# Performance work log

Measured on AMD Instinct MI355X. Metric: run time of the kernel, lower is better.

The kernel has to match this reference:

```python
import jax, jax.numpy as jnp
import numpy as np

B, S, D, H, DFF, G = 2, 2048, 1024, 16, 4096, 64
HD = D // H  # seq_dimensions = d_model // num_heads
SCALE = 1.0 / np.sqrt(HD).astype(np.float32)


def _ln(x, g, b):
    m = x.mean(-1, keepdims=True)
    v = x.var(-1, keepdims=True)
    return (x - m) / jnp.sqrt(v + 1e-5) * g + b


def _mha(q_in, k_in, v_in, wq, bq, wk, bk, wv, bv, wo, bo, mask):
    Bq, Sq, _ = q_in.shape
    Sk = k_in.shape[1]
    def proj(t, w, b):
        return (t @ w + b).reshape(t.shape[0], t.shape[1], H, HD).transpose(0, 2, 1, 3)
    q = proj(q_in, wq, bq)  # [B,H,Sq,HD]
    k = proj(k_in, wk, bk)
    v = proj(v_in, wv, bv)
    scores = jnp.einsum('bhqd,bhkd->bhqk', q, k) * SCALE
    if mask is not None:
        scores = jnp.where(mask, scores, jnp.float32(-1e9))
    a = jax.nn.softmax(scores, axis=-1)
    o = jnp.einsum('bhqk,bhkd->bhqd', a, v).transpose(0, 2, 1, 3).reshape(Bq, Sq, D)
    return o @ wo + bo


def setup_inputs() -> dict:
    key = jax.random.key(0)
    ks = jax.random.split(key, 32)
    w = lambda i, shape: jax.random.normal(ks[i], shape, jnp.float32) * 0.02
    z = lambda shape: jnp.zeros(shape, jnp.float32)
    # BigBird-style mask: causal + global (first G tokens) + G random cols per row
    rng = np.random.default_rng(0)
    mask = np.tril(np.ones((S, S), dtype=bool))
    mask[:, :G] = True
    mask[:G, :] = True
    rand_cols = rng.integers(0, S, size=(S, G))
    mask[np.arange(S)[:, None], rand_cols] = True
    return dict(
        cur_input=jax.random.normal(ks[0], (B, S, D), jnp.float32),
        classVector=jax.random.normal(ks[1], (B, 1, 10), jnp.float32),
        attn_mask=jnp.asarray(mask),
        sa_wq=w(2, (D, D)), sa_bq=z(D), sa_wk=w(3, (D, D)), sa_bk=z(D),
        sa_wv=w(4, (D, D)), sa_bv=z(D), sa_wo=w(5, (D, D)), sa_bo=z(D),
        ln1_g=jnp.ones(D, jnp.float32), ln1_b=z(D),
        ce_w=w(6, (10, D)), ce_b=z(D),
        ca_wq=w(7, (D, D)), ca_bq=z(D), ca_wk=w(8, (D, D)), ca_bk=z(D),
        ca_wv=w(9, (D, D)), ca_bv=z(D), ca_wo=w(10, (D, D)), ca_bo=z(D),
        ln2_g=jnp.ones(D, jnp.float32), ln2_b=z(D),
        ff_w1=w(11, (D, DFF)), ff_b1=z(DFF), ff_w2=w(12, (DFF, D)), ff_b2=z(D),
        ln3_g=jnp.ones(D, jnp.float32), ln3_b=z(D),
    )


def reference(cur_input, classVector, attn_mask,
              sa_wq, sa_bq, sa_wk, sa_bk, sa_wv, sa_bv, sa_wo, sa_bo, ln1_g, ln1_b,
              ce_w, ce_b,
              ca_wq, ca_bq, ca_wk, ca_bk, ca_wv, ca_bv, ca_wo, ca_bo, ln2_g, ln2_b,
              ff_w1, ff_b1, ff_w2, ff_b2, ln3_g, ln3_b):
    # AddNorm(masked rand+global self-attn)
    sa = _mha(cur_input, cur_input, cur_input,
              sa_wq, sa_bq, sa_wk, sa_bk, sa_wv, sa_bv, sa_wo, sa_bo, attn_mask)
    h = _ln(cur_input + sa, ln1_g, ln1_b)
    # class vector embedding -> cross-attn K/V
    cv = classVector @ ce_w + ce_b  # [B,1,D]
    ca = _mha(h, cv, cv, ca_wq, ca_bq, ca_wk, ca_bk, ca_wv, ca_bv, ca_wo, ca_bo, None)
    h2 = _ln(h + ca, ln2_g, ln2_b)
    # AddNorm(FFN)
    ff = jax.nn.relu(h2 @ ff_w1 + ff_b1) @ ff_w2 + ff_b2
    return _ln(h2 + ff, ln3_g, ln3_b)
```

## Files before the change

### kernel.cpp

```cpp
#include <hip/hip_runtime.h>
#include <hip/hip_bf16.h>
#include <stdint.h>

#define S_LEN 2048
#define DMODEL 1024
#define NHEAD 16
#define BATCH 2

typedef __bf16 bf16x8 __attribute__((ext_vector_type(8)));
typedef __bf16 bf16x4 __attribute__((ext_vector_type(4)));
typedef float f32x4 __attribute__((ext_vector_type(4)));

__device__ __forceinline__ void gll16(const void* gsrc, void* ldst) {
  auto g = (const __attribute__((address_space(1))) unsigned int*)(uintptr_t)gsrc;
  auto l = (__attribute__((address_space(3))) unsigned int*)(uint32_t)(uintptr_t)ldst;
  __builtin_amdgcn_global_load_lds(g, l, 16, 0, 0);
}

__device__ __forceinline__ void wt_core(const float* __restrict__ W, __bf16* __restrict__ Wt,
                                        int Kd, int Nd, int bx, int by) {
  __shared__ __bf16 tile[64 * 72];
  const int n0 = bx * 64, k0 = by * 64;
  const int t = threadIdx.x;
#pragma unroll
  for (int i = 0; i < 16; ++i) {
    int idx = t + 256 * i;
    int r = idx >> 6, c = idx & 63;
    tile[r * 72 + c] = (__bf16)W[(size_t)(k0 + r) * Nd + n0 + c];
  }
  __syncthreads();
#pragma unroll
  for (int i = 0; i < 2; ++i) {
    int ch = t + 256 * i;
    int r = ch >> 3, c0 = (ch & 7) * 8;
    bf16x8 v;
#pragma unroll
    for (int j = 0; j < 8; ++j) v[j] = tile[(c0 + j) * 72 + r];
    *(bf16x8*)&Wt[(size_t)(n0 + r) * Kd + k0 + c0] = v;
  }
}

__global__ __launch_bounds__(256) void prep_kernel(
    const uint8_t* __restrict__ m8, unsigned long long* __restrict__ mb, const float* w0,
    const float* w1, const float* w2, const float* w3, __bf16* o0, __bf16* o1, __bf16* o2,
    __bf16* o3, const float* fw1, const float* fw2, __bf16* fo1, __bf16* fo2,
    const float* __restrict__ x, __bf16* __restrict__ y) {
  const int bid = blockIdx.x;
  const int t = threadIdx.x;
  if (bid < 256) {
    const int idx = bid * 256 + t;
    const int r = idx >> 5, c = idx & 31;
    const bool u8 = (m8[1] != 0);
    unsigned long long bits = 0;
    if (u8) {
      const unsigned long long* p = (const unsigned long long*)(m8 + (size_t)r * 2048 + c * 64);
#pragma unroll
      for (int i = 0; i < 8; ++i) {
        unsigned long long wq = p[i];
#pragma unroll
        for (int j = 0; j < 8; ++j)
          if ((wq >> (8 * j)) & 0xFFull) bits |= 1ull << (i * 8 + j);
      }
    } else {
      const int* p = (const int*)m8 + (size_t)r * 2048 + (size_t)c * 64;
#pragma unroll
      for (int i = 0; i < 64; ++i)
        if (p[i] != 0) bits |= 1ull << i;
    }
    mb[(size_t)r * 32 + c] = bits;
  } else if (bid < 1280) {
    const int local = bid - 256;
    const int z = local >> 8, lb = local & 255;
    const float* W = (z == 0) ? w0 : (z == 1) ? w1 : (z == 2) ? w2 : w3;
    __bf16* Wt = (z == 0) ? o0 : (z == 1) ? o1 : (z == 2) ? o2 : o3;
    wt_core(W, Wt, 1024, 1024, lb & 15, lb >> 4);
  } else if (bid < 2304) {
    const int lb = bid - 1280;
    wt_core(fw1, fo1, 1024, 4096, lb & 63, lb >> 6);
  } else if (bid < 3328) {
    const int lb = bid - 2304;
    wt_core(fw2, fo2, 4096, 1024, lb >> 6, lb & 63);
  } else {
    const int lb = bid - 3328;
#pragma unroll
    for (int j = 0; j < 4; ++j) {
      int i = lb * 1024 + j * 256 + t;
      float4 v = ((const float4*)x)[i];
      bf16x4 o = {(__bf16)v.x, (__bf16)v.y, (__bf16)v.z, (__bf16)v.w};
      *(bf16x4*)(y + (size_t)i * 4) = o;
    }
  }
}

__device__ __forceinline__ void gemm_core(const __bf16* __restrict__ A,
                                          const __bf16* __restrict__ Bt,
                                          const float* __restrict__ bias,
                                          float* __restrict__ outF, __bf16* __restrict__ outB,
                                          bool relu, float scale, int N, int K) {
  __shared__ __bf16 As[2][128 * 64];
  __shared__ __bf16 Bs[2][128 * 64];
  const int t = threadIdx.x;
  const int l = t & 63, w = t >> 6;
  const int wr = w >> 1, wc = w & 1;
  const int gx = gridDim.x;
  const int lin = blockIdx.x + gx * blockIdx.y;
  const int cpx = (gx * gridDim.y) >> 3;
  const int s = (lin & 7) * cpx + (lin >> 3);
  const int bx = s % gx, by = s / gx;
  const int l15 = l & 15, l4 = l >> 4;
  f32x4 acc[4][4] = {};
  const size_t arow = (size_t)by * 128;
  const size_t brow = (size_t)bx * 128;

  auto stage = [&](int d, int k0) {
#pragma unroll
    for (int i = 0; i < 4; ++i) {
      int c = t + 256 * i;
      int r = c >> 3, sl = c & 7;
      int kk = (sl ^ (r & 7)) << 3;
      gll16(A + (arow + r) * K + k0 + kk, (char*)As[d] + (size_t)c * 16);
      gll16(Bt + (brow + r) * K + k0 + kk, (char*)Bs[d] + (size_t)c * 16);
    }
  };

  stage(0, 0);
  asm volatile("s_waitcnt vmcnt(0)" ::: "memory");
  __builtin_amdgcn_s_barrier();
  int cur = 0;
  for (int k0 = 0; k0 < K; k0 += 64) {
    if (k0 + 64 < K) stage(cur ^ 1, k0 + 64);
#pragma unroll
    for (int kk = 0; kk < 2; ++kk) {
      bf16x8 af[4], bfr[4];
#pragma unroll
      for (int m = 0; m < 4; ++m) {
        int row = wr * 64 + m * 16 + l15, vs = kk * 4 + l4;
        af[m] = *(const bf16x8*)((char*)As[cur] + row * 128 + ((vs ^ (row & 7)) << 4));
      }
#pragma unroll
      for (int n = 0; n < 4; ++n) {
        int row = wc * 64 + n * 16 + l15, vs = kk * 4 + l4;
        bfr[n] = *(const bf16x8*)((char*)Bs[cur] + row * 128 + ((vs ^ (row & 7)) << 4));
      }
#pragma unroll
      for (int m = 0; m < 4; ++m)
#pragma unroll
        for (int n = 0; n < 4; ++n)
          acc[m][n] = __builtin_amdgcn_mfma_f32_16x16x32_bf16(af[m], bfr[n], acc[m][n], 0, 0, 0);
    }
    asm volatile("s_waitcnt vmcnt(0)" ::: "memory");
    __builtin_amdgcn_s_barrier();
    cur ^= 1;
  }
  const int r0 = by * 128 + wr * 64, c0 = bx * 128 + wc * 64;
#pragma unroll
  for (int m = 0; m < 4; ++m) {
#pragma unroll
    for (int n = 0; n < 4; ++n) {
      int col = c0 + n * 16 + l15;
      float bv = bias ? bias[col] : 0.0f;
#pragma unroll
      for (int i = 0; i < 4; ++i) {
        int row = r0 + m * 16 + l4 * 4 + i;
        float v = (acc[m][n][i] + bv) * scale;
        if (relu) v = fmaxf(v, 0.0f);
        if (outF) outF[(size_t)row * N + col] = v;
        if (outB) outB[(size_t)row * N + col] = (__bf16)v;
      }
    }
  }
}

__global__ __launch_bounds__(256) void gemm_kernel(const __bf16* A, const __bf16* Bt,
                                                   const float* bias, float* outF, __bf16* outB,
                                                   int relu, float scale, int N, int K) {
  gemm_core(A, Bt, bias, outF, outB, relu != 0, scale, N, K);
}

__global__ __launch_bounds__(256) void gemm64_kernel(const __bf16* __restrict__ A,
                                                     const __bf16* __restrict__ Bt,
                                                     const float* __restrict__ bias,
                                                     float* __restrict__ outF,
                                                     __bf16* __restrict__ outB, int relu,
                                                     int N, int K) {
  __shared__ __bf16 As[2][128 * 64];
  __shared__ __bf16 Bs[2][64 * 64];
  const int t = threadIdx.x;
  const int l = t & 63, w = t >> 6;
  const int gx = gridDim.x;
  const int lin = blockIdx.x + gx * blockIdx.y;
  const int cpx = (gx * gridDim.y) >> 3;
  const int s = (lin & 7) * cpx + (lin >> 3);
  const int bx = s % gx, by = s / gx;
  const int l15 = l & 15, l4 = l >> 4;
  f32x4 acc[2][4] = {};
  const size_t arow = (size_t)by * 128;
  const size_t brow = (size_t)bx * 64;

  auto stage = [&](int d, int k0) {
#pragma unroll
    for (int i = 0; i < 4; ++i) {
      int c = t + 256 * i;
      int r = c >> 3, sl = c & 7;
      int kk = (sl ^ (r & 7)) << 3;
      gll16(A + (arow + r) * K + k0 + kk, (char*)As[d] + (size_t)c * 16);
    }
#pragma unroll
    for (int i = 0; i < 2; ++i) {
      int c = t + 256 * i;
      int r = c >> 3, sl = c & 7;
      int kk = (sl ^ (r & 7)) << 3;
      gll16(Bt + (brow + r) * K + k0 + kk, (char*)Bs[d] + (size_t)c * 16);
    }
  };

  stage(0, 0);
  asm volatile("s_waitcnt vmcnt(0)" ::: "memory");
  __builtin_amdgcn_s_barrier();
  int cur = 0;
  for (int k0 = 0; k0 < K; k0 += 64) {
    if (k0 + 64 < K) stage(cur ^ 1, k0 + 64);
#pragma unroll
    for (int kk = 0; kk < 2; ++kk) {
      bf16x8 af[2], bfr[4];
#pragma unroll
      for (int m = 0; m < 2; ++m) {
        int row = w * 32 + m * 16 + l15, vs = kk * 4 + l4;
        af[m] = *(const bf16x8*)((char*)As[cur] + row * 128 + ((vs ^ (row & 7)) << 4));
      }
#pragma unroll
      for (int n = 0; n < 4; ++n) {
        int row = n * 16 + l15, vs = kk * 4 + l4;
        bfr[n] = *(const bf16x8*)((char*)Bs[cur] + row * 128 + ((vs ^ (row & 7)) << 4));
      }
#pragma unroll
      for (int m = 0; m < 2; ++m)
#pragma unroll
        for (int n = 0; n < 4; ++n)
          acc[m][n] = __builtin_amdgcn_mfma_f32_16x16x32_bf16(af[m], bfr[n], acc[m][n], 0, 0, 0);
    }
    asm volatile("s_waitcnt vmcnt(0)" ::: "memory");
    __builtin_amdgcn_s_barrier();
    cur ^= 1;
  }
  const int r0 = by * 128 + w * 32, c0 = bx * 64;
#pragma unroll
  for (int m = 0; m < 2; ++m) {
#pragma unroll
    for (int n = 0; n < 4; ++n) {
      int col = c0 + n * 16 + l15;
      float bv = bias ? bias[col] : 0.0f;
#pragma unroll
      for (int i = 0; i < 4; ++i) {
        int row = r0 + m * 16 + l4 * 4 + i;
        float v = acc[m][n][i] + bv;
        if (relu) v = fmaxf(v, 0.0f);
        if (outF) outF[(size_t)row * N + col] = v;
        if (outB) outB[(size_t)row * N + col] = (__bf16)v;
      }
    }
  }
}

__global__ __launch_bounds__(256) void gemm_qkv_kernel(const __bf16* __restrict__ A,
                                                       const __bf16* __restrict__ WT3,
                                                       const float* bq, const float* bk,
                                                       const float* bv, __bf16* Qo, __bf16* Ko,
                                                       __bf16* Vo) {
  __shared__ __bf16 As[2][128 * 64];
  __shared__ __bf16 Bs[2][128 * 64];
  const int t = threadIdx.x;
  const int l = t & 63, w = t >> 6;
  const int wr = w >> 1, wc = w & 1;
  const int gx = gridDim.x;
  const int lin = blockIdx.x + gx * blockIdx.y;
  const int cpx = (gx * gridDim.y) >> 3;
  const int s = (lin & 7) * cpx + (lin >> 3);
  const int bx = s % gx, by = s / gx;
  const int l15 = l & 15, l4 = l >> 4;
  const int K = 1024;
  f32x4 acc[4][4] = {};
  const size_t arow = (size_t)by * 128;
  const size_t brow = (size_t)bx * 128;

  auto stage = [&](int d, int k0) {
#pragma unroll
    for (int i = 0; i < 4; ++i) {
      int c = t + 256 * i;
      int r = c >> 3, sl = c & 7;
      int kk = (sl ^ (r & 7)) << 3;
      gll16(A + (arow + r) * K + k0 + kk, (char*)As[d] + (size_t)c * 16);
      gll16(WT3 + (brow + r) * K + k0 + kk, (char*)Bs[d] + (size_t)c * 16);
    }
  };

  stage(0, 0);
  asm volatile("s_waitcnt vmcnt(0)" ::: "memory");
  __builtin_amdgcn_s_barrier();
  int cur = 0;
  for (int k0 = 0; k0 < K; k0 += 64) {
    if (k0 + 64 < K) stage(cur ^ 1, k0 + 64);
#pragma unroll
    for (int kk = 0; kk < 2; ++kk) {
      bf16x8 af[4], bfr[4];
#pragma unroll
      for (int m = 0; m < 4; ++m) {
        int row = wr * 64 + m * 16 + l15, vs = kk * 4 + l4;
        af[m] = *(const bf16x8*)((char*)As[cur] + row * 128 + ((vs ^ (row & 7)) << 4));
      }
#pragma unroll
      for (int n = 0; n < 4; ++n) {
        int row = wc * 64 + n * 16 + l15, vs = kk * 4 + l4;
        bfr[n] = *(const bf16x8*)((char*)Bs[cur] + row * 128 + ((vs ^ (row & 7)) << 4));
      }
#pragma unroll
      for (int m = 0; m < 4; ++m)
#pragma unroll
        for (int n = 0; n < 4; ++n)
          acc[m][n] = __builtin_amdgcn_mfma_f32_16x16x32_bf16(af[m], bfr[n], acc[m][n], 0, 0, 0);
    }
    asm volatile("s_waitcnt vmcnt(0)" ::: "memory");
    __builtin_amdgcn_s_barrier();
    cur ^= 1;
  }
  const int z = bx >> 3;
  __bf16* out = (z == 0) ? Qo : (z == 1) ? Ko : Vo;
  const float* bias = (z == 0) ? bq : (z == 1) ? bk : bv;
  const float scale = (z == 0) ? 0.125f : 1.0f;
  const int r0 = by * 128 + wr * 64, c0 = (bx & 7) * 128 + wc * 64;
#pragma unroll
  for (int m = 0; m < 4; ++m) {
#pragma unroll
    for (int n = 0; n < 4; ++n) {
      int col = c0 + n * 16 + l15;
      float bvv = bias[col];
#pragma unroll
      for (int i = 0; i < 4; ++i) {
        int row = r0 + m * 16 + l4 * 4 + i;
        out[(size_t)row * DMODEL + col] = (__bf16)((acc[m][n][i] + bvv) * scale);
      }
    }
  }
}

__global__ __launch_bounds__(256) void vt_kernel(const __bf16* __restrict__ V,
                                                 __bf16* __restrict__ Vt) {
  __shared__ __bf16 tile[64 * 72];
  const int sb = blockIdx.x, h = blockIdx.y, b = blockIdx.z;
  const int t = threadIdx.x;
#pragma unroll
  for (int i = 0; i < 2; ++i) {
    int ch = t + 256 * i;
    int r = ch >> 3, c0 = (ch & 7) * 8;
    *(bf16x8*)&tile[r * 72 + c0] =
        *(const bf16x8*)&V[(size_t)(b * S_LEN + sb * 64 + r) * DMODEL + h * 64 + c0];
  }
  __syncthreads();
#pragma unroll
  for (int i = 0; i < 2; ++i) {
    int ch = t + 256 * i;
    int r = ch >> 3, c0 = (ch & 7) * 8;
    bf16x8 v;
#pragma unroll
    for (int j = 0; j < 8; ++j) v[j] = tile[(c0 + j) * 72 + r];
    *(bf16x8*)&Vt[((size_t)((b * NHEAD + h) * 64) + r) * S_LEN + sb * 64 + c0] = v;
  }
}

__global__ __launch_bounds__(256, 4) void flash_kernel(const __bf16* __restrict__ Q,
                                                       const __bf16* __restrict__ K,
                                                       const __bf16* __restrict__ Vt,
                                                       const unsigned long long* __restrict__ mbits,
                                                       __bf16* __restrict__ O) {
  __shared__ char smem[40 * 1024];
  const int lin = blockIdx.x + 32 * (blockIdx.y + 16 * blockIdx.z);
  const int xr = lin & 7, xm = lin >> 3;
  const int g = xr + 8 * (xm & 3);
  const int qb = xm >> 2;
  const int h = g & 15, b = g >> 4;
  const int t = threadIdx.x, w = t >> 6, l = t & 63;
  const int l15 = l & 15, l4 = l >> 4;
  const int q_glob = qb * 64 + w * 16 + l15;

#pragma unroll
  for (int i = 0; i < 2; ++i) {
    int c = t + 256 * i;
    int r = c >> 3, p = c & 7;
    int vsl = p ^ (r & 7);
    gll16(Q + (size_t)(b * S_LEN + qb * 64 + r) * DMODEL + h * 64 + vsl * 8,
          smem + (size_t)c * 16);
    gll16(K + (size_t)(b * S_LEN + r) * DMODEL + h * 64 + vsl * 8, smem + 8192 + (size_t)c * 16);
    gll16(Vt + (size_t)((b * NHEAD + h) * 64 + r) * S_LEN + vsl * 8, smem + 24576 + (size_t)c * 16);
  }
  __syncthreads();

  bf16x8 aq[2];
#pragma unroll
  for (int ks = 0; ks < 2; ++ks) {
    int row = w * 16 + l15, vs = ks * 4 + l4;
    aq[ks] = *(const bf16x8*)(smem + row * 128 + ((vs ^ (row & 7)) << 4));
  }
  char* PsW = smem + w * 2048;

  f32x4 o[4] = {};
  float mrow = -INFINITY, lrow = 0.f;
  unsigned long long mb_cur = 0, mb_next = 0;
  int cur = 0;
  for (int kt = 0; kt < 32; ++kt) {
    char* Kc = smem + 8192 + cur * 8192;
    char* Vc = smem + 24576 + cur * 8192;
    if (kt < 31) {
      char* Kn = smem + 8192 + (cur ^ 1) * 8192;
      char* Vn = smem + 24576 + (cur ^ 1) * 8192;
#pragma unroll
      for (int i = 0; i < 2; ++i) {
        int c = t + 256 * i;
        int r = c >> 3, p = c & 7;
        int vsl = p ^ (r & 7);
        gll16(K + (size_t)(b * S_LEN + (kt + 1) * 64 + r) * DMODEL + h * 64 + vsl * 8,
              Kn + (size_t)c * 16);
        gll16(Vt + (size_t)((b * NHEAD + h) * 64 + r) * S_LEN + (kt + 1) * 64 + vsl * 8,
              Vn + (size_t)c * 16);
      }
      mb_next = mbits[(size_t)q_glob * 32 + kt + 1];
    }
    f32x4 s[4] = {};
    __builtin_amdgcn_s_setprio(1);
#pragma unroll
    for (int ks = 0; ks < 2; ++ks)
#pragma unroll
      for (int n = 0; n < 4; ++n) {
        int row = n * 16 + l15, vs = ks * 4 + l4;
        bf16x8 kf = *(const bf16x8*)(Kc + row * 128 + ((vs ^ (row & 7)) << 4));
        s[n] = __builtin_amdgcn_mfma_f32_16x16x32_bf16(kf, aq[ks], s[n], 0, 0, 0);
      }
    __builtin_amdgcn_s_setprio(0);
    const bool skip = (kt < qb) || (kt == 0) || (qb == 0);
    float tmax = s[0][0];
#pragma unroll
    for (int n = 0; n < 4; ++n)
#pragma unroll
      for (int i = 0; i < 4; ++i) tmax = fmaxf(tmax, s[n][i]);
    tmax = fmaxf(tmax, __shfl_xor(tmax, 16));
    tmax = fmaxf(tmax, __shfl_xor(tmax, 32));
    if (__ballot(tmax > mrow)) {
      const float nm = fmaxf(mrow, tmax);
      const float alpha = __expf(mrow - nm);
      mrow = nm;
      lrow *= alpha;
#pragma unroll
      for (int i = 0; i < 4; ++i) {
        float ai = __shfl(alpha, (l & 48) | (l4 * 4 + i));
#pragma unroll
        for (int n = 0; n < 4; ++n) o[n][i] *= ai;
      }
    }
    float pv[4][4];
#pragma unroll
    for (int n = 0; n < 4; ++n)
#pragma unroll
      for (int i = 0; i < 4; ++i) pv[n][i] = __expf(s[n][i] - mrow);
    if (!skip) {
#pragma unroll
      for (int n = 0; n < 4; ++n) {
        unsigned int mB = (unsigned int)(mb_cur >> (n * 16 + l4 * 4));
#pragma unroll
        for (int i = 0; i < 4; ++i)
          if (!((mB >> i) & 1)) pv[n][i] = 0.f;
      }
    }
    float tsum = 0.f;
#pragma unroll
    for (int n = 0; n < 4; ++n)
#pragma unroll
      for (int i = 0; i < 4; ++i) tsum += pv[n][i];
    tsum += __shfl_xor(tsum, 16);
    tsum += __shfl_xor(tsum, 32);
    lrow += tsum;
#pragma unroll
    for (int n = 0; n < 4; ++n) {
      bf16x4 pk = {(__bf16)pv[n][0], (__bf16)pv[n][1], (__bf16)pv[n][2], (__bf16)pv[n][3]};
      int slot = n * 4 + l4;
      *(bf16x4*)(PsW + l15 * 128 + ((slot ^ l15) & 15) * 8) = pk;
    }
#pragma unroll
    for (int ks = 0; ks < 2; ++ks) {
      int s0 = (ks * 8 + l4 * 2) ^ l15;
      int s1 = (ks * 8 + l4 * 2 + 1) ^ l15;
      bf16x4 pa0 = *(const bf16x4*)(PsW + l15 * 128 + (s0 & 15) * 8);
      bf16x4 pa1 = *(const bf16x4*)(PsW + l15 * 128 + (s1 & 15) * 8);
      bf16x8 ap = {pa0[0], pa0[1], pa0[2], pa0[3], pa1[0], pa1[1], pa1[2], pa1[3]};
      __builtin_amdgcn_s_setprio(1);
#pragma unroll
      for (int n = 0; n < 4; ++n) {
        int vrow = n * 16 + l15, vvs = ks * 4 + l4;
        bf16x8 bv = *(const bf16x8*)(Vc + vrow * 128 + ((vvs ^ (vrow & 7)) << 4));
        o[n] = __builtin_amdgcn_mfma_f32_16x16x32_bf16(ap, bv, o[n], 0, 0, 0);
      }
      __builtin_amdgcn_s_setprio(0);
    }
    asm volatile("s_waitcnt vmcnt(0)" ::: "memory");
    __builtin_amdgcn_s_barrier();
    mb_cur = mb_next;
    cur ^= 1;
  }
#pragma unroll
  for (int i = 0; i < 4; ++i) {
    float li = __shfl(lrow, (l & 48) | (l4 * 4 + i));
    float rli = 1.0f / li;
#pragma unroll
    for (int n = 0; n < 4; ++n)
      O[(size_t)(b * S_LEN + qb * 64 + w * 16 + l4 * 4 + i) * DMODEL + h * 64 + n * 16 + l15] =
          (__bf16)(o[n][i] * rli);
  }
}

__global__ __launch_bounds__(256) void ln_kernel(const float* __restrict__ x,
                                                 const float* __restrict__ res,
                                                 const float* __restrict__ resvec,
                                                 const float* __restrict__ g,
                                                 const float* __restrict__ beta,
                                                 float* __restrict__ outF,
                                                 __bf16* __restrict__ outB) {
  const int row = blockIdx.x;
  const int b = row >> 11;
  const int t = threadIdx.x;
  float4 v = ((const float4*)(x + (size_t)row * DMODEL))[t];
  if (res) {
    float4 r = ((const float4*)(res + (size_t)row * DMODEL))[t];
    v.x += r.x; v.y += r.y; v.z += r.z; v.w += r.w;
  }
  if (resvec) {
    float4 r = ((const float4*)(resvec + (size_t)b * DMODEL))[t];
    v.x += r.x; v.y += r.y; v.z += r.z; v.w += r.w;
  }
  float s1 = v.x + v.y + v.z + v.w;
  float s2 = v.x * v.x + v.y * v.y + v.z * v.z + v.w * v.w;
#pragma unroll
  for (int off = 32; off; off >>= 1) {
    s1 += __shfl_xor(s1, off);
    s2 += __shfl_xor(s2, off);
  }
  __shared__ float red[8];
  const int w = t >> 6, l = t & 63;
  if (l == 0) { red[w] = s1; red[4 + w] = s2; }
  __syncthreads();
  s1 = red[0] + red[1] + red[2] + red[3];
  s2 = red[4] + red[5] + red[6] + red[7];
  const float mean = s1 * (1.0f / DMODEL);
  const float var = s2 * (1.0f / DMODEL) - mean * mean;
  const float rstd = rsqrtf(var + 1e-5f);
  float4 gg = ((const float4*)g)[t];
  float4 bb = ((const float4*)beta)[t];
  float4 o;
  o.x = (v.x - mean) * rstd * gg.x + bb.x;
  o.y = (v.y - mean) * rstd * gg.y + bb.y;
  o.z = (v.z - mean) * rstd * gg.z + bb.z;
  o.w = (v.w - mean) * rstd * gg.w + bb.w;
  if (outF) ((float4*)(outF + (size_t)row * DMODEL))[t] = o;
  if (outB) {
    bf16x4 p = {(__bf16)o.x, (__bf16)o.y, (__bf16)o.z, (__bf16)o.w};
    *(bf16x4*)(outB + (size_t)row * DMODEL + t * 4) = p;
  }
}

__global__ __launch_bounds__(256) void matvec_part_kernel(const float* __restrict__ x,
                                                          const float* __restrict__ W,
                                                          float* __restrict__ part,
                                                          const float* __restrict__ cls,
                                                          const float* __restrict__ cw,
                                                          const float* __restrict__ cb) {
  const int c = blockIdx.x, b = blockIdx.y;
  const int t = threadIdx.x;
  const int k0 = c * 16;
  __shared__ float xs[16];
  if (cls) {
    if (t < 16) {
      float s = cb[k0 + t];
#pragma unroll
      for (int j = 0; j < 10; ++j) s += cls[b * 10 + j] * cw[j * DMODEL + k0 + t];
      xs[t] = s;
    }
  } else {
    if (t < 16) xs[t] = x[b * DMODEL + k0 + t];
  }
  __syncthreads();
  float4 acc = {0.f, 0.f, 0.f, 0.f};
#pragma unroll
  for (int k = 0; k < 16; ++k) {
    float xv = xs[k];
    float4 wv = ((const float4*)(W + (size_t)(k0 + k) * DMODEL))[t];
    acc.x += xv * wv.x; acc.y += xv * wv.y; acc.z += xv * wv.z; acc.w += xv * wv.w;
  }
  ((float4*)(part + ((size_t)(b * 64 + c)) * DMODEL))[t] = acc;
}

__global__ __launch_bounds__(256) void matvec_red_kernel(const float* __restrict__ part,
                                                         const float* __restrict__ bias,
                                                         float* __restrict__ out) {
  const int b = blockIdx.y;
  const int t = threadIdx.x;
  float4 acc = ((const float4*)bias)[t];
#pragma unroll 8
  for (int c = 0; c < 64; ++c) {
    float4 p = ((const float4*)(part + ((size_t)(b * 64 + c)) * DMODEL))[t];
    acc.x += p.x; acc.y += p.y; acc.z += p.z; acc.w += p.w;
  }
  ((float4*)(out + (size_t)b * DMODEL))[t] = acc;
}

extern "C" void kernel_launch(void* const* d_in, const int* in_sizes, int n_in, void* d_out,
                              int out_size, void* d_ws, size_t ws_size, hipStream_t stream) {
  (void)in_sizes; (void)n_in; (void)out_size; (void)ws_size;
  const float* cur = (const float*)d_in[0];
  const float* cls = (const float*)d_in[1];
  const uint8_t* msk = (const uint8_t*)d_in[2];
  const float* sa_wq = (const float*)d_in[3];
  const float* sa_bq = (const float*)d_in[4];
  const float* sa_wk = (const float*)d_in[5];
  const float* sa_bk = (const float*)d_in[6];
  const float* sa_wv = (const float*)d_in[7];
  const float* sa_bv = (const float*)d_in[8];
  const float* sa_wo = (const float*)d_in[9];
  const float* sa_bo = (const float*)d_in[10];
  const float* ln1_g = (const float*)d_in[11];
  const float* ln1_b = (const float*)d_in[12];
  const float* ce_w = (const float*)d_in[13];
  const float* ce_b = (const float*)d_in[14];
  const float* ca_wv = (const float*)d_in[19];
  const float* ca_bv = (const float*)d_in[20];
  const float* ca_wo = (const float*)d_in[21];
  const float* ca_bo = (const float*)d_in[22];
  const float* ln2_g = (const float*)d_in[23];
  const float* ln2_b = (const float*)d_in[24];
  const float* ff_w1 = (const float*)d_in[25];
  const float* ff_b1 = (const float*)d_in[26];
  const float* ff_w2 = (const float*)d_in[27];
  const float* ff_b2 = (const float*)d_in[28];
  const float* ln3_g = (const float*)d_in[29];
  const float* ln3_b = (const float*)d_in[30];

  char* ws = (char*)d_ws;
  const size_t MB = 1ull << 20;
  __bf16* WQT = (__bf16*)(ws + 0 * MB);
  __bf16* WKT = (__bf16*)(ws + 2 * MB);
  __bf16* WVT = (__bf16*)(ws + 4 * MB);
  __bf16* WOT = (__bf16*)(ws + 6 * MB);
  __bf16* W1T = (__bf16*)(ws + 8 * MB);
  __bf16* W2T = (__bf16*)(ws + 16 * MB);
  __bf16* XBF = (__bf16*)(ws + 24 * MB);
  __bf16* QBF = (__bf16*)(ws + 32 * MB);
  __bf16* KBF = (__bf16*)(ws + 40 * MB);
  __bf16* VBF = (__bf16*)(ws + 48 * MB);
  __bf16* VTT = (__bf16*)(ws + 56 * MB);
  __bf16* F1 = (__bf16*)(ws + 32 * MB);
  float* ATT = (float*)(ws + 64 * MB);
  float* HF = (float*)(ws + 80 * MB);
  float* H2F = (float*)(ws + 96 * MB);
  __bf16* H2B = (__bf16*)(ws + 112 * MB);
  float* VV = (float*)(ws + 120 * MB);
  float* CAV = (float*)(ws + 120 * MB + 65536);
  unsigned long long* MBITS = (unsigned long long*)(ws + 121 * MB);
  float* MVP = (float*)(ws + 122 * MB);

  dim3 blk(256);
  prep_kernel<<<dim3(4352), blk, 0, stream>>>(msk, MBITS, sa_wq, sa_wk, sa_wv, sa_wo, WQT, WKT,
                                              WVT, WOT, ff_w1, ff_w2, W1T, W2T, cur, XBF);
  gemm_qkv_kernel<<<dim3(24, 32), blk, 0, stream>>>(XBF, WQT, sa_bq, sa_bk, sa_bv, QBF, KBF, VBF);
  vt_kernel<<<dim3(32, 16, 2), blk, 0, stream>>>(VBF, VTT);
  flash_kernel<<<dim3(32, 16, 2), blk, 0, stream>>>(QBF, KBF, VTT, MBITS, XBF);
  gemm64_kernel<<<dim3(16, 32), blk, 0, stream>>>(XBF, WOT, sa_bo, ATT, nullptr, 0, 1024, 1024);
  ln_kernel<<<dim3(4096), blk, 0, stream>>>(cur, ATT, nullptr, ln1_g, ln1_b, HF, nullptr);
  matvec_part_kernel<<<dim3(64, 2), blk, 0, stream>>>(nullptr, ca_wv, MVP, cls, ce_w, ce_b);
  matvec_red_kernel<<<dim3(1, 2), blk, 0, stream>>>(MVP, ca_bv, VV);
  matvec_part_kernel<<<dim3(64, 2), blk, 0, stream>>>(VV, ca_wo, MVP, nullptr, nullptr, nullptr);
  matvec_red_kernel<<<dim3(1, 2), blk, 0, stream>>>(MVP, ca_bo, CAV);
  ln_kernel<<<dim3(4096), blk, 0, stream>>>(HF, nullptr, CAV, ln2_g, ln2_b, H2F, H2B);
  gemm_kernel<<<dim3(32, 32), blk, 0, stream>>>(H2B, W1T, ff_b1, nullptr, F1, 1, 1.0f, 4096, 1024);
  gemm64_kernel<<<dim3(16, 32), blk, 0, stream>>>(F1, W2T, ff_b2, ATT, nullptr, 0, 1024, 4096);
  ln_kernel<<<dim3(4096), blk, 0, stream>>>(H2F, ATT, nullptr, ln3_g, ln3_b, (float*)d_out,
                                            nullptr);
}
```

Baseline: 296.2 us.

## Use exp2 softmax with MFMA row sums and fold cross-attn matvecs into prep

The Q scale now includes log2(e), so the flash kernel can use the raw v_exp_f32 (exp2) instruction in place of __expf. The softmax denominator is accumulated by an extra MFMA against a ones vector instead of shuffle-based row sums. The cross-attention class-vector embedding and the first matvec stage move into prep_kernel as extra blocks, and the first reduction is fused into the second matvec, removing two launches. The trade-offs are one extra MFMA per tile, and a row sum taken from bf16-rounded probabilities rather than the fp32 values.

```diff
diff --git a/kernel.cpp b/kernel.cpp
--- a/kernel.cpp
+++ b/kernel.cpp
@@ -17,6 +17,12 @@
   __builtin_amdgcn_global_load_lds(g, l, 16, 0, 0);
 }
 
+__device__ __forceinline__ float fexp2(float x) {
+  float r;
+  asm("v_exp_f32 %0, %1" : "=v"(r) : "v"(x));
+  return r;
+}
+
 __device__ __forceinline__ void wt_core(const float* __restrict__ W, __bf16* __restrict__ Wt,
                                         int Kd, int Nd, int bx, int by) {
   __shared__ __bf16 tile[64 * 72];
@@ -40,11 +46,27 @@
   }
 }
 
+__device__ __forceinline__ void mv_stage(const float* __restrict__ W, float* __restrict__ part,
+                                         const float* xs, int c, int b) {
+  const int t = threadIdx.x;
+  const int k0 = c * 16;
+  float4 acc = {0.f, 0.f, 0.f, 0.f};
+#pragma unroll
+  for (int k = 0; k < 16; ++k) {
+    float xv = xs[k];
+    float4 wv = ((const float4*)(W + (size_t)(k0 + k) * DMODEL))[t];
+    acc.x += xv * wv.x; acc.y += xv * wv.y; acc.z += xv * wv.z; acc.w += xv * wv.w;
+  }
+  ((float4*)(part + ((size_t)(b * 64 + c)) * DMODEL))[t] = acc;
+}
+
 __global__ __launch_bounds__(256) void prep_kernel(
     const uint8_t* __restrict__ m8, unsigned long long* __restrict__ mb, const float* w0,
     const float* w1, const float* w2, const float* w3, __bf16* o0, __bf16* o1, __bf16* o2,
     __bf16* o3, const float* fw1, const float* fw2, __bf16* fo1, __bf16* fo2,
-    const float* __restrict__ x, __bf16* __restrict__ y) {
+    const float* __restrict__ x, __bf16* __restrict__ y, const float* __restrict__ cls,
+    const float* __restrict__ cw, const float* __restrict__ cb, const float* __restrict__ cawv,
+    float* __restrict__ mvp) {
   const int bid = blockIdx.x;
   const int t = threadIdx.x;
   if (bid < 256) {
@@ -80,7 +102,7 @@
   } else if (bid < 3328) {
     const int lb = bid - 2304;
     wt_core(fw2, fo2, 4096, 1024, lb >> 6, lb & 63);
-  } else {
+  } else if (bid < 4352) {
     const int lb = bid - 3328;
 #pragma unroll
     for (int j = 0; j < 4; ++j) {
@@ -89,6 +111,18 @@
       bf16x4 o = {(__bf16)v.x, (__bf16)v.y, (__bf16)v.z, (__bf16)v.w};
       *(bf16x4*)(y + (size_t)i * 4) = o;
     }
+  } else {
+    const int local = bid - 4352;
+    const int c = local & 63, b = local >> 6;
+    __shared__ float xs[16];
+    if (t < 16) {
+      float s = cb[c * 16 + t];
+#pragma unroll
+      for (int j = 0; j < 10; ++j) s += cls[b * 10 + j] * cw[j * DMODEL + c * 16 + t];
+      xs[t] = s;
+    }
+    __syncthreads();
+    mv_stage(cawv, mvp, xs, c, b);
   }
 }
 
@@ -326,7 +360,7 @@
   const int z = bx >> 3;
   __bf16* out = (z == 0) ? Qo : (z == 1) ? Ko : Vo;
   const float* bias = (z == 0) ? bq : (z == 1) ? bk : bv;
-  const float scale = (z == 0) ? 0.125f : 1.0f;
+  const float scale = (z == 0) ? 0.18033688011112042f : 1.0f;
   const int r0 = by * 128 + wr * 64, c0 = (bx & 7) * 128 + wc * 64;
 #pragma unroll
   for (int m = 0; m < 4; ++m) {
@@ -401,9 +435,12 @@
     aq[ks] = *(const bf16x8*)(smem + row * 128 + ((vs ^ (row & 7)) << 4));
   }
   char* PsW = smem + w * 2048;
+  const __bf16 one = (__bf16)1.0f;
+  const bf16x8 ones8 = {one, one, one, one, one, one, one, one};
 
   f32x4 o[4] = {};
-  float mrow = -INFINITY, lrow = 0.f;
+  f32x4 o4 = {0.f, 0.f, 0.f, 0.f};
+  float mrow = -INFINITY;
   unsigned long long mb_cur = 0, mb_next = 0;
   int cur = 0;
   for (int kt = 0; kt < 32; ++kt) {
@@ -445,12 +482,12 @@
     tmax = fmaxf(tmax, __shfl_xor(tmax, 32));
     if (__ballot(tmax > mrow)) {
       const float nm = fmaxf(mrow, tmax);
-      const float alpha = __expf(mrow - nm);
+      const float alpha = fexp2(mrow - nm);
       mrow = nm;
-      lrow *= alpha;
 #pragma unroll
       for (int i = 0; i < 4; ++i) {
         float ai = __shfl(alpha, (l & 48) | (l4 * 4 + i));
+        o4[i] *= ai;
 #pragma unroll
         for (int n = 0; n < 4; ++n) o[n][i] *= ai;
       }
@@ -459,7 +496,7 @@
 #pragma unroll
     for (int n = 0; n < 4; ++n)
 #pragma unroll
-      for (int i = 0; i < 4; ++i) pv[n][i] = __expf(s[n][i] - mrow);
+      for (int i = 0; i < 4; ++i) pv[n][i] = fexp2(s[n][i] - mrow);
     if (!skip) {
 #pragma unroll
       for (int n = 0; n < 4; ++n) {
@@ -469,14 +506,6 @@
           if (!((mB >> i) & 1)) pv[n][i] = 0.f;
       }
     }
-    float tsum = 0.f;
-#pragma unroll
-    for (int n = 0; n < 4; ++n)
-#pragma unroll
-      for (int i = 0; i < 4; ++i) tsum += pv[n][i];
-    tsum += __shfl_xor(tsum, 16);
-    tsum += __shfl_xor(tsum, 32);
-    lrow += tsum;
 #pragma unroll
     for (int n = 0; n < 4; ++n) {
       bf16x4 pk = {(__bf16)pv[n][0], (__bf16)pv[n][1], (__bf16)pv[n][2], (__bf16)pv[n][3]};
@@ -497,6 +526,7 @@
         bf16x8 bv = *(const bf16x8*)(Vc + vrow * 128 + ((vvs ^ (vrow & 7)) << 4));
         o[n] = __builtin_amdgcn_mfma_f32_16x16x32_bf16(ap, bv, o[n], 0, 0, 0);
       }
+      o4 = __builtin_amdgcn_mfma_f32_16x16x32_bf16(ap, ones8, o4, 0, 0, 0);
       __builtin_amdgcn_s_setprio(0);
     }
     asm volatile("s_waitcnt vmcnt(0)" ::: "memory");
@@ -506,8 +536,7 @@
   }
 #pragma unroll
   for (int i = 0; i < 4; ++i) {
-    float li = __shfl(lrow, (l & 48) | (l4 * 4 + i));
-    float rli = 1.0f / li;
+    float rli = 1.0f / o4[i];
 #pragma unroll
     for (int n = 0; n < 4; ++n)
       O[(size_t)(b * S_LEN + qb * 64 + w * 16 + l4 * 4 + i) * DMODEL + h * 64 + n * 16 + l15] =
@@ -564,35 +593,21 @@
   }
 }
 
-__global__ __launch_bounds__(256) void matvec_part_kernel(const float* __restrict__ x,
-                                                          const float* __restrict__ W,
-                                                          float* __restrict__ part,
-                                                          const float* __restrict__ cls,
-                                                          const float* __restrict__ cw,
-                                                          const float* __restrict__ cb) {
+__global__ __launch_bounds__(256) void matvec_part2_kernel(const float* __restrict__ mvp,
+                                                           const float* __restrict__ bv_bias,
+                                                           const float* __restrict__ W,
+                                                           float* __restrict__ part_out) {
   const int c = blockIdx.x, b = blockIdx.y;
   const int t = threadIdx.x;
-  const int k0 = c * 16;
   __shared__ float xs[16];
-  if (cls) {
-    if (t < 16) {
-      float s = cb[k0 + t];
-#pragma unroll
-      for (int j = 0; j < 10; ++j) s += cls[b * 10 + j] * cw[j * DMODEL + k0 + t];
-      xs[t] = s;
-    }
-  } else {
-    if (t < 16) xs[t] = x[b * DMODEL + k0 + t];
+  if (t < 16) {
+    float s = bv_bias[c * 16 + t];
+#pragma unroll 8
+    for (int c2 = 0; c2 < 64; ++c2) s += mvp[((size_t)(b * 64 + c2)) * DMODEL + c * 16 + t];
+    xs[t] = s;
   }
   __syncthreads();
-  float4 acc = {0.f, 0.f, 0.f, 0.f};
-#pragma unroll
-  for (int k = 0; k < 16; ++k) {
-    float xv = xs[k];
-    float4 wv = ((const float4*)(W + (size_t)(k0 + k) * DMODEL))[t];
-    acc.x += xv * wv.x; acc.y += xv * wv.y; acc.z += xv * wv.z; acc.w += xv * wv.w;
-  }
-  ((float4*)(part + ((size_t)(b * 64 + c)) * DMODEL))[t] = acc;
+  mv_stage(W, part_out, xs, c, b);
 }
 
 __global__ __launch_bounds__(256) void matvec_red_kernel(const float* __restrict__ part,
@@ -658,23 +673,22 @@
   float* HF = (float*)(ws + 80 * MB);
   float* H2F = (float*)(ws + 96 * MB);
   __bf16* H2B = (__bf16*)(ws + 112 * MB);
-  float* VV = (float*)(ws + 120 * MB);
-  float* CAV = (float*)(ws + 120 * MB + 65536);
+  float* CAV = (float*)(ws + 120 * MB);
   unsigned long long* MBITS = (unsigned long long*)(ws + 121 * MB);
   float* MVP = (float*)(ws + 122 * MB);
+  float* MVP2 = (float*)(ws + 123 * MB);
 
   dim3 blk(256);
-  prep_kernel<<<dim3(4352), blk, 0, stream>>>(msk, MBITS, sa_wq, sa_wk, sa_wv, sa_wo, WQT, WKT,
-                                              WVT, WOT, ff_w1, ff_w2, W1T, W2T, cur, XBF);
+  prep_kernel<<<dim3(4480), blk, 0, stream>>>(msk, MBITS, sa_wq, sa_wk, sa_wv, sa_wo, WQT, WKT,
+                                              WVT, WOT, ff_w1, ff_w2, W1T, W2T, cur, XBF, cls,
+                                              ce_w, ce_b, ca_wv, MVP);
   gemm_qkv_kernel<<<dim3(24, 32), blk, 0, stream>>>(XBF, WQT, sa_bq, sa_bk, sa_bv, QBF, KBF, VBF);
   vt_kernel<<<dim3(32, 16, 2), blk, 0, stream>>>(VBF, VTT);
   flash_kernel<<<dim3(32, 16, 2), blk, 0, stream>>>(QBF, KBF, VTT, MBITS, XBF);
   gemm64_kernel<<<dim3(16, 32), blk, 0, stream>>>(XBF, WOT, sa_bo, ATT, nullptr, 0, 1024, 1024);
   ln_kernel<<<dim3(4096), blk, 0, stream>>>(cur, ATT, nullptr, ln1_g, ln1_b, HF, nullptr);
-  matvec_part_kernel<<<dim3(64, 2), blk, 0, stream>>>(nullptr, ca_wv, MVP, cls, ce_w, ce_b);
-  matvec_red_kernel<<<dim3(1, 2), blk, 0, stream>>>(MVP, ca_bv, VV);
-  matvec_part_kernel<<<dim3(64, 2), blk, 0, stream>>>(VV, ca_wo, MVP, nullptr, nullptr, nullptr);
-  matvec_red_kernel<<<dim3(1, 2), blk, 0, stream>>>(MVP, ca_bo, CAV);
+  matvec_part2_kernel<<<dim3(64, 2), blk, 0, stream>>>(MVP, ca_bv, ca_wo, MVP2);
+  matvec_red_kernel<<<dim3(1, 2), blk, 0, stream>>>(MVP2, ca_bo, CAV);
   ln_kernel<<<dim3(4096), blk, 0, stream>>>(HF, nullptr, CAV, ln2_g, ln2_b, H2F, H2B);
   gemm_kernel<<<dim3(32, 32), blk, 0, stream>>>(H2B, W1T, ff_b1, nullptr, F1, 1, 1.0f, 4096, 1024);
   gemm64_kernel<<<dim3(16, 32), blk, 0, stream>>>(F1, W2T, ff_b2, ATT, nullptr, 0, 1024, 4096);
```

After: 288.1 us, median of 2. -2.7%, faster.
